# Optimization experiments

Hardware: AMD Instinct MI355X
Metric: run time of the kernel (lower is better)

Reference implementation:

```python
import jax, jax.numpy as jnp
import numpy as np

B, N_PER, D = 128, 512, 128        # graphs, nodes per graph, feature width
N = B * N_PER                      # 65536 total nodes
E = 524288                         # total edges (avg degree 8)
KS = (410, 328, 263)               # ceil(0.8*512), ceil(0.8*410), ceil(0.8*328)


def setup_inputs() -> dict:
    key = jax.random.key(0)
    ks = jax.random.split(key, 20)
    p = lambda k, shape: jax.random.normal(k, shape, jnp.float32) * 0.05
    rng = np.random.default_rng(0)
    g = rng.integers(0, B, size=E)
    s = rng.integers(0, N_PER, size=E)
    t = rng.integers(0, N_PER, size=E)
    edge_index = jnp.asarray(np.stack([g * N_PER + s, g * N_PER + t]).astype(np.int32))
    inp = {
        'x': jax.random.normal(ks[0], (N, 1, D), jnp.float32),
        'edge_index': edge_index,
    }
    i = 1
    for l in (1, 2, 3):
        inp[f'conv{l}_wl'] = p(ks[i], (D, D)); i += 1   # SAGEConv lin_l (neighbors) weight
        inp[f'conv{l}_bl'] = p(ks[i], (D,));  i += 1   # SAGEConv lin_l bias
        inp[f'conv{l}_wr'] = p(ks[i], (D, D)); i += 1   # SAGEConv lin_r (root) weight
        inp[f'pool{l}_w'] = p(ks[i], (D,));   i += 1   # TopKPooling score vector
    inp['lin1_w'] = p(ks[13], (128, 256)); inp['lin1_b'] = p(ks[14], (128,))
    inp['lin2_w'] = p(ks[15], (64, 128));  inp['lin2_b'] = p(ks[16], (64,))
    inp['lin3_w'] = p(ks[17], (1, 64));    inp['lin3_b'] = p(ks[18], (1,))
    return inp


def _sage(x, node_mask, src, dst, wl, bl, wr):
    # SAGEConv, mean aggregation: lin_l(mean_{j->i} x_j) + lin_r(x_i)
    em = (node_mask[src] & node_mask[dst]).astype(x.dtype)   # [E] valid-edge mask
    msum = jax.ops.segment_sum(x[src] * em[:, None], dst, num_segments=N)
    deg = jax.ops.segment_sum(em, dst, num_segments=N)
    mean = msum / jnp.maximum(deg, 1.0)[:, None]
    return mean @ wl.T + bl + x @ wr.T


def _topk_pool(x, node_mask, w, k):
    # TopKPooling: score = x.w/||w||; keep top-k per graph; gate kept x by tanh(score)
    score = (x @ w) / (jnp.linalg.norm(w) + 1e-16)           # [N]
    score = jnp.where(node_mask, score, -jnp.inf)
    _, idx = jax.lax.top_k(score.reshape(B, N_PER), k)       # [B, k] within-graph ids
    nm = jnp.zeros((B, N_PER), bool).at[jnp.arange(B)[:, None], idx].set(True).reshape(-1)
    x = jnp.where(nm[:, None], x * jnp.tanh(score)[:, None], 0.0)
    return x, nm


def _readout(x, node_mask, k):
    # cat([global_max_pool, global_mean_pool]) over the k surviving nodes per graph
    xb = x.reshape(B, N_PER, -1)
    mb = node_mask.reshape(B, N_PER, 1)
    gmax = jnp.max(jnp.where(mb, xb, -jnp.inf), axis=1)
    gmean = jnp.sum(jnp.where(mb, xb, 0.0), axis=1) / k
    return jnp.concatenate([gmax, gmean], axis=1)            # [B, 2D]


def _forward(edge_index, x, conv1_wl, conv1_bl, conv1_wr, pool1_w,
             conv2_wl, conv2_bl, conv2_wr, pool2_w,
             conv3_wl, conv3_bl, conv3_wr, pool3_w,
             lin1_w, lin1_b, lin2_w, lin2_b, lin3_w, lin3_b):
    src, dst = edge_index[0], edge_index[1]
    h = x[:, 0, :]                                           # x.squeeze(1) -> [N, D]
    nm = jnp.ones((N,), bool)
    layers = ((conv1_wl, conv1_bl, conv1_wr, pool1_w),
              (conv2_wl, conv2_bl, conv2_wr, pool2_w),
              (conv3_wl, conv3_bl, conv3_wr, pool3_w))
    reads = []
    for (wl, bl, wr, pw), k in zip(layers, KS):
        h = jax.nn.relu(_sage(h, nm, src, dst, wl, bl, wr))
        h, nm = _topk_pool(h, nm, pw, k)
        reads.append(_readout(h, nm, float(k)))
    z = reads[0] + reads[1] + reads[2]                       # [B, 256]
    z = jax.nn.relu(z @ lin1_w.T + lin1_b)
    z = jax.nn.relu(z @ lin2_w.T + lin2_b)
    # dropout p=0.5 is a no-op at eval time
    return jax.nn.sigmoid(z @ lin3_w.T + lin3_b)[:, 0]       # [B]


def reference(x, edge_index, conv1_wl, conv1_bl, conv1_wr, pool1_w,
              conv2_wl, conv2_bl, conv2_wr, pool2_w,
              conv3_wl, conv3_bl, conv3_wr, pool3_w,
              lin1_w, lin1_b, lin2_w, lin2_b, lin3_w, lin3_b):
    return _forward(edge_index, x, conv1_wl, conv1_bl, conv1_wr, pool1_w,
                    conv2_wl, conv2_bl, conv2_wr, pool2_w,
                    conv3_wl, conv3_bl, conv3_wr, pool3_w,
                    lin1_w, lin1_b, lin2_w, lin2_b, lin3_w, lin3_b)
```

## Files before the change

kernel.cpp:

```cpp
#include <hip/hip_runtime.h>
#include <math.h>

#define NND 65536
#define NPER 512
#define NGR 128
#define DD 128
#define NED 524288

typedef __attribute__((ext_vector_type(8))) short short8;
typedef __attribute__((ext_vector_type(4))) float f32x4;

__device__ __forceinline__ unsigned short f2b(float f) {
  unsigned u = __float_as_uint(f);
  return (unsigned short)((u + 0x7FFFu + ((u >> 16) & 1u)) >> 16);
}
__device__ __forceinline__ float b2f(unsigned short h) {
  return __uint_as_float(((unsigned)h) << 16);
}


__global__ __launch_bounds__(256) void init_prepw_kernel(
    int* __restrict__ counts, float2* __restrict__ tm,
    const float* __restrict__ wl0, const float* __restrict__ wr0,
    const float* __restrict__ wl1, const float* __restrict__ wr1,
    const float* __restrict__ wl2, const float* __restrict__ wr2,
    unsigned short* __restrict__ Whi, unsigned short* __restrict__ Wlo) {
  const int bid = blockIdx.x;
  if (bid < 256) {
    int i = bid * 256 + threadIdx.x;
    counts[i] = 0;
    tm[i] = make_float2(1.f, 1.f);
    return;
  }
  const float* wls[3] = {wl0, wl1, wl2};
  const float* wrs[3] = {wr0, wr1, wr2};
  int e = (bid - 256) * 256 + threadIdx.x;
  int l = e >> 15;
  int o = e & 32767;
  int j = o & 7;
  int lane = (o >> 3) & 63;
  int nt = (o >> 9) & 7;
  int kc = o >> 12;
  int li = lane & 15, q = lane >> 4;
  int n = nt * 16 + li;
  int k = kc * 32 + q * 8 + j;
  const float* src = (k < 128) ? wls[l] : wrs[l];
  float v = src[n * DD + (k & 127)];
  unsigned short hi = f2b(v);
  float lo = v - b2f(hi);
  Whi[e] = hi;
  Wlo[e] = f2b(lo);
}

__global__ __launch_bounds__(256) void hist_kernel(const int* __restrict__ ei,
                                                   int* __restrict__ counts) {
  int e = blockIdx.x * 256 + threadIdx.x;
  atomicAdd(&counts[ei[NED + e]], 1);
}


__global__ __launch_bounds__(256) void scan1_kernel(const int* __restrict__ counts,
                                                    int* __restrict__ csum) {
  __shared__ int ws[4];
  const int b = blockIdx.x;
  const int t = threadIdx.x;
  const int4 v = ((const int4*)(counts + b * 1024))[t];
  int s = v.x + v.y + v.z + v.w;
#pragma unroll
  for (int o = 32; o > 0; o >>= 1) s += __shfl_down(s, o);
  if ((t & 63) == 0) ws[t >> 6] = s;
  __syncthreads();
  if (t == 0) csum[b] = ws[0] + ws[1] + ws[2] + ws[3];
}

__global__ __launch_bounds__(256) void scan2_kernel(const int* __restrict__ counts,
                                                    const int* __restrict__ csum,
                                                    int* __restrict__ off,
                                                    int* __restrict__ cursor) {
  __shared__ int s_part[256];
  __shared__ int s_base;
  const int b = blockIdx.x;
  const int t = threadIdx.x;
  const int4 v = ((const int4*)(counts + b * 1024))[t];
  const int s = v.x + v.y + v.z + v.w;
  s_part[t] = s;
  if (t < 64) {
    int val = (t < b) ? csum[t] : 0;
#pragma unroll
    for (int o = 32; o > 0; o >>= 1) val += __shfl_down(val, o);
    if (t == 0) s_base = val;
  }
  __syncthreads();
  for (int d = 1; d < 256; d <<= 1) {
    int val = (t >= d) ? s_part[t - d] : 0;
    __syncthreads();
    s_part[t] += val;
    __syncthreads();
  }
  const int excl = s_base + ((t == 0) ? 0 : s_part[t - 1]);
  int4 o4;
  o4.x = excl;
  o4.y = excl + v.x;
  o4.z = o4.y + v.y;
  o4.w = o4.z + v.z;
  ((int4*)(off + b * 1024))[t] = o4;
  ((int4*)(cursor + b * 1024))[t] = o4;
  if (b == 0 && t == 0) off[NND] = NED;
}

__global__ __launch_bounds__(256) void scatter_kernel(const int* __restrict__ ei,
                                                      int* __restrict__ cursor,
                                                      int* __restrict__ ssrc) {
  int e = blockIdx.x * 256 + threadIdx.x;
  int dst = ei[NED + e];
  int pos = atomicAdd(&cursor[dst], 1);
  ssrc[pos] = ei[e];
}


template <int CM>
__global__ __launch_bounds__(256) void agg_kernel_t(const float* __restrict__ x,
                                                    const float2* __restrict__ tm,
                                                    const int* __restrict__ off,
                                                    const int* __restrict__ ssrc,
                                                    unsigned short* __restrict__ mhi,
                                                    unsigned short* __restrict__ mlo) {
  const int wave = threadIdx.x >> 6;
  const int lane = threadIdx.x & 63;
  const int half = lane >> 5;
  const int l = lane & 31;
  const int bid = blockIdx.x;
  const int xcd = bid & 7;
  const int slot = bid >> 3;
  const int graph = xcd * 16 + (slot >> 5);
  const int within = slot & 31;
  const int d0 = graph * NPER + within * 16 + wave * 4;

  int offv = 0;
  if (lane < 5) offv = off[d0 + lane];
  float deadv = 1.f;
  if (CM && lane < 4) deadv = tm[d0 + lane].x;
  const int b0 = __shfl(offv, 0);
  const int b1 = __shfl(offv, 1);
  const int b2 = __shfl(offv, 2);
  const int b3 = __shfl(offv, 3);
  const int e3 = __shfl(offv, 4);
  float dd[4];
  if (CM) {
    dd[0] = __shfl(deadv, 0);
    dd[1] = __shfl(deadv, 1);
    dd[2] = __shfl(deadv, 2);
    dd[3] = __shfl(deadv, 3);
  }
  const int begs[4] = {b0, b1, b2, b3};
  const int ends[4] = {b1, b2, b3, e3};

  float4 acc[4];
  int deg[4];
#pragma unroll
  for (int d = 0; d < 4; ++d) {
    acc[d] = make_float4(0.f, 0.f, 0.f, 0.f);
    deg[d] = 0;
  }

  for (int base = b0; base < e3; base += 64) {
    const int nwin = min(64, e3 - base);
    int sv = 0;
    float tv = 0.f;
    int live = 0;
    if (lane < nwin) {
      sv = ssrc[base + lane];
      if (CM) {
        const float2 mt = tm[sv];
        live = (mt.x != 0.f);
        tv = mt.y;
      }
    }
    unsigned long long bl;
    if (CM)
      bl = __ballot(live);
    else
      bl = (nwin == 64) ? ~0ull : ((1ull << nwin) - 1);

#pragma unroll
    for (int d = 0; d < 4; ++d) {
      if (CM && dd[d] == 0.f) continue;
      const int lo = max(begs[d], base);
      const int hi = min(ends[d], base + 64);
      if (lo >= hi) continue;
      const int j0 = lo - base;
      const int j1 = hi - base;
      const unsigned long long wm =
          (((j1 == 64) ? ~0ull : ((1ull << j1) - 1)) & ~((1ull << j0) - 1));
      deg[d] += (int)__popcll(bl & wm);
      int j = j0 + half;
      for (; j + 6 < j1; j += 8) {
        const int s0 = __shfl(sv, j);
        const int s1 = __shfl(sv, j + 2);
        const int s2 = __shfl(sv, j + 4);
        const int s3 = __shfl(sv, j + 6);
        const float4 v0 = *(const float4*)(x + (size_t)s0 * DD + l * 4);
        const float4 v1 = *(const float4*)(x + (size_t)s1 * DD + l * 4);
        const float4 v2 = *(const float4*)(x + (size_t)s2 * DD + l * 4);
        const float4 v3 = *(const float4*)(x + (size_t)s3 * DD + l * 4);
        if (CM) {
          const float t0 = __shfl(tv, j), t1 = __shfl(tv, j + 2);
          const float t2 = __shfl(tv, j + 4), t3 = __shfl(tv, j + 6);
          acc[d].x += v0.x * t0 + v1.x * t1 + v2.x * t2 + v3.x * t3;
          acc[d].y += v0.y * t0 + v1.y * t1 + v2.y * t2 + v3.y * t3;
          acc[d].z += v0.z * t0 + v1.z * t1 + v2.z * t2 + v3.z * t3;
          acc[d].w += v0.w * t0 + v1.w * t1 + v2.w * t2 + v3.w * t3;
        } else {
          acc[d].x += v0.x + v1.x + v2.x + v3.x;
          acc[d].y += v0.y + v1.y + v2.y + v3.y;
          acc[d].z += v0.z + v1.z + v2.z + v3.z;
          acc[d].w += v0.w + v1.w + v2.w + v3.w;
        }
      }
      for (; j < j1; j += 2) {
        const int s = __shfl(sv, j);
        const float4 v = *(const float4*)(x + (size_t)s * DD + l * 4);
        if (CM) {
          const float t = __shfl(tv, j);
          acc[d].x += v.x * t;
          acc[d].y += v.y * t;
          acc[d].z += v.z * t;
          acc[d].w += v.w * t;
        } else {
          acc[d].x += v.x;
          acc[d].y += v.y;
          acc[d].z += v.z;
          acc[d].w += v.w;
        }
      }
    }
  }

#pragma unroll
  for (int d = 0; d < 4; ++d) {
    float4 a = acc[d];
    a.x += __shfl(a.x, lane ^ 32);
    a.y += __shfl(a.y, lane ^ 32);
    a.z += __shfl(a.z, lane ^ 32);
    a.w += __shfl(a.w, lane ^ 32);
    if (lane < 32) {
      const float inv = 1.f / (float)max(deg[d], 1);
      float4 m;
      m.x = a.x * inv;
      m.y = a.y * inv;
      m.z = a.z * inv;
      m.w = a.w * inv;
      ushort4 hv, lv;
      hv.x = f2b(m.x); lv.x = f2b(m.x - b2f(hv.x));
      hv.y = f2b(m.y); lv.y = f2b(m.y - b2f(hv.y));
      hv.z = f2b(m.z); lv.z = f2b(m.z - b2f(hv.z));
      hv.w = f2b(m.w); lv.w = f2b(m.w - b2f(hv.w));
      const size_t ad = (size_t)(d0 + d) * DD + l * 4;
      *(ushort4*)(mhi + ad) = hv;
      *(ushort4*)(mlo + ad) = lv;
    }
  }
}


#define GBM 64

template <int SCALE>
__global__ __launch_bounds__(256) void gemm_kernel_t(
    const unsigned short* __restrict__ Amh, const unsigned short* __restrict__ Aml,
    const float* __restrict__ Ax, const float2* __restrict__ tmp,
    const unsigned short* __restrict__ Whi, const unsigned short* __restrict__ Wlo,
    const float* __restrict__ bias, const float* __restrict__ pw,
    float* __restrict__ outp, float* __restrict__ sraw) {
  __shared__ short Ah[4096];
  __shared__ short Al[4096];
  __shared__ float s_sp[4][GBM];
  const int tid = threadIdx.x;
  const int wv = tid >> 6;
  const int lane = tid & 63;
  const int q = lane >> 4;
  const int li = lane & 15;
  const int row0 = blockIdx.x * GBM;

  int sdst[2];
#pragma unroll
  for (int i = 0; i < 2; ++i) {
    const int id = tid + i * 256;
    const int r = id >> 3;
    const int kb = (id & 7) << 2;
    sdst[i] = ((r >> 4) * 64 + (kb >> 3) * 16 + (r & 15)) * 8 + (kb & 7);
  }

  f32x4 acc[4][2];
#pragma unroll
  for (int m = 0; m < 4; ++m)
#pragma unroll
    for (int n = 0; n < 2; ++n) acc[m][n] = (f32x4){0.f, 0.f, 0.f, 0.f};

  float4 pa[2];
  ushort4 pmh[2], pml[2];
  short8 pbh[2], pbl[2];

#define LOADA(KC)                                                                      \
  {                                                                                    \
    if ((KC) < 4) {                                                                    \
      const int cb = (KC)*32;                                                          \
      _Pragma("unroll") for (int i = 0; i < 2; ++i) {                                  \
        const int id = tid + i * 256;                                                  \
        const size_t ga = (size_t)(row0 + (id >> 3)) * DD + cb + ((id & 7) << 2);      \
        pmh[i] = *(const ushort4*)(Amh + ga);                                          \
        pml[i] = *(const ushort4*)(Aml + ga);                                          \
      }                                                                                \
    } else {                                                                           \
      const int cb = ((KC)&3) * 32;                                                    \
      _Pragma("unroll") for (int i = 0; i < 2; ++i) {                                  \
        const int id = tid + i * 256;                                                  \
        pa[i] = *(const float4*)(Ax + (size_t)(row0 + (id >> 3)) * DD + cb + ((id & 7) << 2)); \
        if (SCALE) {                                                                   \
          const float tt = tmp[row0 + (id >> 3)].y;                                    \
          pa[i].x *= tt; pa[i].y *= tt; pa[i].z *= tt; pa[i].w *= tt;                  \
        }                                                                              \
      }                                                                                \
    }                                                                                  \
  }
#define LOADB(KC)                                                                      \
  {                                                                                    \
    _Pragma("unroll") for (int n = 0; n < 2; ++n) {                                    \
      const int ga = (((KC)*8 + wv * 2 + n) * 64 + lane) * 8;                          \
      pbh[n] = *(const short8*)(Whi + ga);                                             \
      pbl[n] = *(const short8*)(Wlo + ga);                                             \
    }                                                                                  \
  }
#define STAGE(KC)                                                                      \
  {                                                                                    \
    short* Adh = Ah + ((KC)&1) * 2048;                                                 \
    short* Adl = Al + ((KC)&1) * 2048;                                                 \
    if ((KC) < 4) {                                                                    \
      _Pragma("unroll") for (int i = 0; i < 2; ++i) {                                  \
        *(ushort4*)(Adh + sdst[i]) = pmh[i];                                           \
        *(ushort4*)(Adl + sdst[i]) = pml[i];                                           \
      }                                                                                \
    } else {                                                                           \
      _Pragma("unroll") for (int i = 0; i < 2; ++i) {                                  \
        ushort4 hv, lv;                                                                \
        hv.x = f2b(pa[i].x); lv.x = f2b(pa[i].x - b2f(hv.x));                          \
        hv.y = f2b(pa[i].y); lv.y = f2b(pa[i].y - b2f(hv.y));                          \
        hv.z = f2b(pa[i].z); lv.z = f2b(pa[i].z - b2f(hv.z));                          \
        hv.w = f2b(pa[i].w); lv.w = f2b(pa[i].w - b2f(hv.w));                          \
        *(ushort4*)(Adh + sdst[i]) = hv;                                               \
        *(ushort4*)(Adl + sdst[i]) = lv;                                               \
      }                                                                                \
    }                                                                                  \
  }

  LOADA(0) LOADB(0)
  STAGE(0)
  LOADA(1)

#pragma unroll
  for (int kc = 0; kc < 8; ++kc) {
    short8 bh[2], bl[2];
    bh[0] = pbh[0]; bh[1] = pbh[1];
    bl[0] = pbl[0]; bl[1] = pbl[1];
    __syncthreads();
    short8 ah[4], al[4];
    const short* Ash = Ah + (kc & 1) * 2048;
    const short* Asl = Al + (kc & 1) * 2048;
#pragma unroll
    for (int m = 0; m < 4; ++m) {
      ah[m] = *(const short8*)(Ash + (m * 64 + lane) * 8);
      al[m] = *(const short8*)(Asl + (m * 64 + lane) * 8);
    }
    switch (kc) {
      case 0: STAGE(1) LOADB(1) LOADA(2) break;
      case 1: STAGE(2) LOADB(2) LOADA(3) break;
      case 2: STAGE(3) LOADB(3) LOADA(4) break;
      case 3: STAGE(4) LOADB(4) LOADA(5) break;
      case 4: STAGE(5) LOADB(5) LOADA(6) break;
      case 5: STAGE(6) LOADB(6) LOADA(7) break;
      case 6: STAGE(7) LOADB(7) break;
      default: break;
    }
#pragma unroll
    for (int m = 0; m < 4; ++m)
#pragma unroll
      for (int n = 0; n < 2; ++n) {
        acc[m][n] = __builtin_amdgcn_mfma_f32_16x16x32_bf16(ah[m], bh[n], acc[m][n], 0, 0, 0);
        acc[m][n] = __builtin_amdgcn_mfma_f32_16x16x32_bf16(ah[m], bl[n], acc[m][n], 0, 0, 0);
        acc[m][n] = __builtin_amdgcn_mfma_f32_16x16x32_bf16(al[m], bh[n], acc[m][n], 0, 0, 0);
      }
  }
#undef LOADA
#undef LOADB
#undef STAGE

  const int c0 = wv * 32 + li;
  const int c1 = wv * 32 + 16 + li;
  const float b0 = bias[c0], b1 = bias[c1];
  const float p0 = pw[c0], p1 = pw[c1];
  float sp[16];
#pragma unroll
  for (int m = 0; m < 4; ++m) {
#pragma unroll
    for (int i = 0; i < 4; ++i) {
      const int r = row0 + m * 16 + q * 4 + i;
      const float v0 = fmaxf(acc[m][0][i] + b0, 0.f);
      const float v1 = fmaxf(acc[m][1][i] + b1, 0.f);
      outp[(size_t)r * DD + c0] = v0;
      outp[(size_t)r * DD + c1] = v1;
      sp[m * 4 + i] = v0 * p0 + v1 * p1;
    }
  }
#pragma unroll
  for (int e = 0; e < 16; ++e) {
    sp[e] += __shfl_xor(sp[e], 1);
    sp[e] += __shfl_xor(sp[e], 2);
    sp[e] += __shfl_xor(sp[e], 4);
    sp[e] += __shfl_xor(sp[e], 8);
  }
  if (li == 0) {
#pragma unroll
    for (int e = 0; e < 16; ++e) s_sp[wv][(e >> 2) * 16 + q * 4 + (e & 3)] = sp[e];
  }
  __syncthreads();
  if (tid < GBM)
    sraw[row0 + tid] = s_sp[0][tid] + s_sp[1][tid] + s_sp[2][tid] + s_sp[3][tid];
}


__global__ __launch_bounds__(256) void pool_kernel(const float* __restrict__ h,
                                                   const float* __restrict__ sraw,
                                                   const float* __restrict__ pw,
                                                   const float2* __restrict__ tmP,
                                                   float2* __restrict__ tmN,
                                                   float* __restrict__ zp,
                                                   const int kk) {
  __shared__ float s_sc[NPER];
  __shared__ float s_t[128];
  __shared__ unsigned char s_sel[128];
  __shared__ int s_rk[256];
  __shared__ float4 red4[512];
  __shared__ float s_norm;
  const int b = blockIdx.x;
  const int g = b >> 2;
  const int q = b & 3;
  const int tid = threadIdx.x;
  const int lane = tid & 63;

  if (tid < 64) {
    const float v0 = pw[lane], v1 = pw[lane + 64];
    float p = v0 * v0 + v1 * v1;
#pragma unroll
    for (int o = 32; o > 0; o >>= 1) p += __shfl_down(p, o);
    if (lane == 0) s_norm = 1.f / (sqrtf(p) + 1e-16f);
  }
  __syncthreads();
  const float inv_norm = s_norm;
#pragma unroll
  for (int i = 0; i < 2; ++i) {
    const int n = tid + i * 256;
    const int node = g * NPER + n;
    s_sc[n] = (tmP[node].x != 0.f) ? sraw[node] * inv_norm : -INFINITY;
  }
  __syncthreads();

  {
    const int n = q * 128 + (tid & 127);
    const int jb = (tid >> 7) * 256;
    const float s = s_sc[n];
    int rank = 0;
    for (int j = jb; j < jb + 256; ++j) {
      const float sj = s_sc[j];
      rank += (sj > s || (sj == s && j < n)) ? 1 : 0;
    }
    s_rk[tid] = rank;
  }
  __syncthreads();
  if (tid < 128) {
    const int n = q * 128 + tid;
    const int rank = s_rk[tid] + s_rk[tid + 128];
    const int sel = (rank < kk) ? 1 : 0;
    const float s = s_sc[n];
    const float t = sel ? tanhf(s) : 0.f;
    tmN[g * NPER + n] = make_float2(sel ? 1.f : 0.f, t);
    s_sel[tid] = (unsigned char)sel;
    s_t[tid] = t;
  }
  __syncthreads();

  const int c = tid & 31;
  const int r = tid >> 5;
  float4 pmax = make_float4(-INFINITY, -INFINITY, -INFINITY, -INFINITY);
  float4 psum = make_float4(0.f, 0.f, 0.f, 0.f);
  const size_t nbase = (size_t)g * NPER + q * 128;
  const float4* h4 = (const float4*)h;
  for (int i = 0; i < 16; ++i) {
    const int nl = r + 8 * i;
    if (s_sel[nl]) {
      float4 v = h4[(nbase + nl) * 32 + c];
      const float t = s_t[nl];
      v.x *= t; v.y *= t; v.z *= t; v.w *= t;
      pmax.x = fmaxf(pmax.x, v.x);
      pmax.y = fmaxf(pmax.y, v.y);
      pmax.z = fmaxf(pmax.z, v.z);
      pmax.w = fmaxf(pmax.w, v.w);
      psum.x += v.x; psum.y += v.y; psum.z += v.z; psum.w += v.w;
    }
  }
  red4[r * 32 + c] = pmax;
  red4[256 + r * 32 + c] = psum;
  __syncthreads();
  if (tid < 32) {
    float4 m = red4[tid];
    float4 sm = red4[256 + tid];
#pragma unroll
    for (int rr = 1; rr < 8; ++rr) {
      const float4 a = red4[rr * 32 + tid];
      const float4 s2 = red4[256 + rr * 32 + tid];
      m.x = fmaxf(m.x, a.x); m.y = fmaxf(m.y, a.y);
      m.z = fmaxf(m.z, a.z); m.w = fmaxf(m.w, a.w);
      sm.x += s2.x; sm.y += s2.y; sm.z += s2.z; sm.w += s2.w;
    }
    *(float4*)(zp + (size_t)b * 256 + tid * 4) = m;
    *(float4*)(zp + (size_t)b * 256 + 128 + tid * 4) = sm;
  }
}


__global__ __launch_bounds__(128) void mlp_kernel(const float* __restrict__ zpart,
                                                  const float* __restrict__ w1,
                                                  const float* __restrict__ b1,
                                                  const float* __restrict__ w2,
                                                  const float* __restrict__ b2,
                                                  const float* __restrict__ w3,
                                                  const float* __restrict__ b3,
                                                  float* __restrict__ out,
                                                  const float ik0, const float ik1,
                                                  const float ik2) {
  __shared__ float z[256];
  __shared__ float h1[128];
  __shared__ float h2[64];
  const int g = blockIdx.x;
  const int t = threadIdx.x;
  const float iks[3] = {ik0, ik1, ik2};
  float zmax = 0.f, zmean = 0.f;
#pragma unroll
  for (int l = 0; l < 3; ++l) {
    const float* zp = zpart + ((size_t)l * 512 + g * 4) * 256;
    zmax += fmaxf(fmaxf(zp[t], zp[256 + t]), fmaxf(zp[512 + t], zp[768 + t]));
    zmean += (zp[128 + t] + zp[384 + t] + zp[640 + t] + zp[896 + t]) * iks[l];
  }
  z[t] = zmax;
  z[128 + t] = zmean;
  __syncthreads();
  float a = b1[t];
  for (int k = 0; k < 256; ++k) a = fmaf(z[k], w1[t * 256 + k], a);
  h1[t] = fmaxf(a, 0.f);
  __syncthreads();
  if (t < 64) {
    float a2 = b2[t];
    for (int k = 0; k < 128; ++k) a2 = fmaf(h1[k], w2[t * 128 + k], a2);
    h2[t] = fmaxf(a2, 0.f);
  }
  __syncthreads();
  if (t == 0) {
    float a3 = b3[0];
    for (int k = 0; k < 64; ++k) a3 = fmaf(h2[k], w3[k], a3);
    out[g] = 1.f / (1.f + expf(-a3));
  }
}


extern "C" void kernel_launch(void* const* d_in, const int* in_sizes, int n_in,
                              void* d_out, int out_size, void* d_ws, size_t ws_size,
                              hipStream_t stream) {
  (void)in_sizes; (void)n_in; (void)out_size; (void)ws_size;
  const float* x_in = (const float*)d_in[0];
  const int* ei = (const int*)d_in[1];
  const float* wl[3] = {(const float*)d_in[2], (const float*)d_in[6], (const float*)d_in[10]};
  const float* cbl[3] = {(const float*)d_in[3], (const float*)d_in[7], (const float*)d_in[11]};
  const float* wr[3] = {(const float*)d_in[4], (const float*)d_in[8], (const float*)d_in[12]};
  const float* pw[3] = {(const float*)d_in[5], (const float*)d_in[9], (const float*)d_in[13]};
  const float* l1w = (const float*)d_in[14];
  const float* l1b = (const float*)d_in[15];
  const float* l2w = (const float*)d_in[16];
  const float* l2b = (const float*)d_in[17];
  const float* l3w = (const float*)d_in[18];
  const float* l3b = (const float*)d_in[19];
  float* out = (float*)d_out;

  char* w = (char*)d_ws;
  int* counts = (int*)(w + 0 * (1 << 20));
  int* off = (int*)(w + 1 * (1 << 20));
  int* csum = (int*)(w + 1 * (1 << 20) + (1 << 19));
  int* cursor = (int*)(w + 2 * (1 << 20));
  float* sraw = (float*)(w + 2 * (1 << 20));
  float2* tmA = (float2*)(w + 3 * (1 << 20));
  float2* tmB = (float2*)(w + 3 * (1 << 20) + (1 << 19));
  float* zpart = (float*)(w + 4 * (1 << 20));
  unsigned short* Whi = (unsigned short*)(w + 5 * (1 << 20) + (1 << 19));
  unsigned short* Wlo = (unsigned short*)(w + 5 * (1 << 20) + 3 * (1 << 18));
  int* ssrc = (int*)(w + 6 * (1 << 20));
  unsigned short* mhi = (unsigned short*)(w + (size_t)8 * (1 << 20));
  unsigned short* mlo = (unsigned short*)(w + (size_t)24 * (1 << 20));
  float* hA = (float*)(w + (size_t)40 * (1 << 20));
  float* hB = (float*)(w + (size_t)72 * (1 << 20));

  init_prepw_kernel<<<640, 256, 0, stream>>>(counts, tmA, wl[0], wr[0], wl[1], wr[1],
                                             wl[2], wr[2], Whi, Wlo);
  hist_kernel<<<NED / 256, 256, 0, stream>>>(ei, counts);
  scan1_kernel<<<64, 256, 0, stream>>>(counts, csum);
  scan2_kernel<<<64, 256, 0, stream>>>(counts, csum, off, cursor);
  scatter_kernel<<<NED / 256, 256, 0, stream>>>(ei, cursor, ssrc);

  const int ks[3] = {410, 328, 263};
  const float* xl = x_in;
  float* houts[3] = {hA, hB, hA};
  float2* tprev[3] = {tmA, tmB, tmA};
  float2* tnext[3] = {tmB, tmA, tmB};
  for (int l = 0; l < 3; ++l) {
    float* hout = houts[l];
    if (l == 0) {
      agg_kernel_t<0><<<4096, 256, 0, stream>>>(xl, tprev[l], off, ssrc, mhi, mlo);
      gemm_kernel_t<0><<<NND / GBM, 256, 0, stream>>>(mhi, mlo, xl, tprev[l],
                                                      Whi + (size_t)l * 32768,
                                                      Wlo + (size_t)l * 32768, cbl[l], pw[l],
                                                      hout, sraw);
    } else {
      agg_kernel_t<1><<<4096, 256, 0, stream>>>(xl, tprev[l], off, ssrc, mhi, mlo);
      gemm_kernel_t<1><<<NND / GBM, 256, 0, stream>>>(mhi, mlo, xl, tprev[l],
                                                      Whi + (size_t)l * 32768,
                                                      Wlo + (size_t)l * 32768, cbl[l], pw[l],
                                                      hout, sraw);
    }
    pool_kernel<<<NGR * 4, 256, 0, stream>>>(hout, sraw, pw[l], tprev[l], tnext[l],
                                             zpart + (size_t)l * 512 * 256, ks[l]);
    xl = hout;
  }
  mlp_kernel<<<NGR, 128, 0, stream>>>(zpart, l1w, l1b, l2w, l2b, l3w, l3b, out,
                                      1.f / 410.f, 1.f / 328.f, 1.f / 263.f);
}
```

Baseline: 362.9 us.

## Stage per-graph feature half-tile in LDS for neighbor aggregation

The aggregation kernel now assigns one 1024-thread block to each graph and half of the feature columns. It loads that graph's 512x64 feature slab, the mask/tanh table and the CSR offsets into shared memory, then gathers neighbor rows from LDS instead of global memory, relying on edges staying within a graph (the source index is masked to a local id). This removes scattered global gathers, but uses about 132KB of LDS per block, launches only 256 blocks, and each lane accumulates a single scalar column, so occupancy and parallelism drop.

```diff
diff --git a/kernel.cpp b/kernel.cpp
--- a/kernel.cpp
+++ b/kernel.cpp
@@ -119,146 +119,104 @@
 
 
 template <int CM>
-__global__ __launch_bounds__(256) void agg_kernel_t(const float* __restrict__ x,
-                                                    const float2* __restrict__ tm,
-                                                    const int* __restrict__ off,
-                                                    const int* __restrict__ ssrc,
-                                                    unsigned short* __restrict__ mhi,
-                                                    unsigned short* __restrict__ mlo) {
-  const int wave = threadIdx.x >> 6;
-  const int lane = threadIdx.x & 63;
-  const int half = lane >> 5;
-  const int l = lane & 31;
-  const int bid = blockIdx.x;
-  const int xcd = bid & 7;
-  const int slot = bid >> 3;
-  const int graph = xcd * 16 + (slot >> 5);
-  const int within = slot & 31;
-  const int d0 = graph * NPER + within * 16 + wave * 4;
-
-  int offv = 0;
-  if (lane < 5) offv = off[d0 + lane];
-  float deadv = 1.f;
-  if (CM && lane < 4) deadv = tm[d0 + lane].x;
-  const int b0 = __shfl(offv, 0);
-  const int b1 = __shfl(offv, 1);
-  const int b2 = __shfl(offv, 2);
-  const int b3 = __shfl(offv, 3);
-  const int e3 = __shfl(offv, 4);
-  float dd[4];
+__global__ __launch_bounds__(1024) void agg_kernel_t(const float* __restrict__ x,
+                                                     const float2* __restrict__ tm,
+                                                     const int* __restrict__ off,
+                                                     const int* __restrict__ ssrc,
+                                                     unsigned short* __restrict__ mhi,
+                                                     unsigned short* __restrict__ mlo) {
+  __shared__ float xs[NPER * 64];
+  __shared__ float2 tms[NPER];
+  __shared__ int soff[NPER + 1];
+  const int b = blockIdx.x;
+  const int g = b >> 1;
+  const int colbase = (b & 1) << 6;
+  const int tid = threadIdx.x;
+  const int lane = tid & 63;
+  const int w = tid >> 6;
+  const int nbase = g * NPER;
+
+  {
+    const int row = tid >> 4;
+    const int c4 = (tid & 15) << 2;
+#pragma unroll
+    for (int r = 0; r < NPER; r += 64) {
+      const float4 v =
+          *(const float4*)(x + (size_t)(nbase + row + r) * DD + colbase + c4);
+      *(float4*)(xs + (row + r) * 64 + c4) = v;
+    }
+  }
   if (CM) {
-    dd[0] = __shfl(deadv, 0);
-    dd[1] = __shfl(deadv, 1);
-    dd[2] = __shfl(deadv, 2);
-    dd[3] = __shfl(deadv, 3);
-  }
-  const int begs[4] = {b0, b1, b2, b3};
-  const int ends[4] = {b1, b2, b3, e3};
-
-  float4 acc[4];
-  int deg[4];
-#pragma unroll
-  for (int d = 0; d < 4; ++d) {
-    acc[d] = make_float4(0.f, 0.f, 0.f, 0.f);
-    deg[d] = 0;
-  }
-
-  for (int base = b0; base < e3; base += 64) {
-    const int nwin = min(64, e3 - base);
-    int sv = 0;
-    float tv = 0.f;
-    int live = 0;
-    if (lane < nwin) {
-      sv = ssrc[base + lane];
-      if (CM) {
-        const float2 mt = tm[sv];
-        live = (mt.x != 0.f);
-        tv = mt.y;
-      }
-    }
-    unsigned long long bl;
-    if (CM)
-      bl = __ballot(live);
-    else
-      bl = (nwin == 64) ? ~0ull : ((1ull << nwin) - 1);
-
-#pragma unroll
-    for (int d = 0; d < 4; ++d) {
-      if (CM && dd[d] == 0.f) continue;
-      const int lo = max(begs[d], base);
-      const int hi = min(ends[d], base + 64);
-      if (lo >= hi) continue;
-      const int j0 = lo - base;
-      const int j1 = hi - base;
-      const unsigned long long wm =
-          (((j1 == 64) ? ~0ull : ((1ull << j1) - 1)) & ~((1ull << j0) - 1));
-      deg[d] += (int)__popcll(bl & wm);
-      int j = j0 + half;
-      for (; j + 6 < j1; j += 8) {
-        const int s0 = __shfl(sv, j);
-        const int s1 = __shfl(sv, j + 2);
-        const int s2 = __shfl(sv, j + 4);
-        const int s3 = __shfl(sv, j + 6);
-        const float4 v0 = *(const float4*)(x + (size_t)s0 * DD + l * 4);
-        const float4 v1 = *(const float4*)(x + (size_t)s1 * DD + l * 4);
-        const float4 v2 = *(const float4*)(x + (size_t)s2 * DD + l * 4);
-        const float4 v3 = *(const float4*)(x + (size_t)s3 * DD + l * 4);
+    if (tid < NPER) tms[tid] = tm[nbase + tid];
+  }
+  if (tid < NPER + 1) soff[tid] = off[nbase + tid];
+  __syncthreads();
+
+  const float* xl = xs + lane;
+  for (int i = 0; i < 32; ++i) {
+    const int n = w * 32 + i;
+    if (CM && tms[n].x == 0.f) continue;
+    const int beg = soff[n];
+    const int end = soff[n + 1];
+    float acc = 0.f;
+    int deg = 0;
+    for (int base = beg; base < end; base += 64) {
+      const int cnt = min(64, end - base);
+      int sv = 0;
+      float tv = 0.f;
+      int live = 0;
+      if (lane < cnt) {
+        sv = (ssrc[base + lane] & (NPER - 1)) << 6;
         if (CM) {
-          const float t0 = __shfl(tv, j), t1 = __shfl(tv, j + 2);
-          const float t2 = __shfl(tv, j + 4), t3 = __shfl(tv, j + 6);
-          acc[d].x += v0.x * t0 + v1.x * t1 + v2.x * t2 + v3.x * t3;
-          acc[d].y += v0.y * t0 + v1.y * t1 + v2.y * t2 + v3.y * t3;
-          acc[d].z += v0.z * t0 + v1.z * t1 + v2.z * t2 + v3.z * t3;
-          acc[d].w += v0.w * t0 + v1.w * t1 + v2.w * t2 + v3.w * t3;
-        } else {
-          acc[d].x += v0.x + v1.x + v2.x + v3.x;
-          acc[d].y += v0.y + v1.y + v2.y + v3.y;
-          acc[d].z += v0.z + v1.z + v2.z + v3.z;
-          acc[d].w += v0.w + v1.w + v2.w + v3.w;
+          const float2 mt = tms[sv >> 6];
+          live = (mt.x != 0.f);
+          tv = mt.y;
         }
       }
-      for (; j < j1; j += 2) {
-        const int s = __shfl(sv, j);
-        const float4 v = *(const float4*)(x + (size_t)s * DD + l * 4);
-        if (CM) {
+      if (CM)
+        deg += (int)__popcll(__ballot(live));
+      else
+        deg += cnt;
+      int j = 0;
+      if (CM) {
+        for (; j + 3 < cnt; j += 4) {
+          const int s0 = __shfl(sv, j), s1 = __shfl(sv, j + 1);
+          const int s2 = __shfl(sv, j + 2), s3 = __shfl(sv, j + 3);
+          const float t0 = __shfl(tv, j), t1 = __shfl(tv, j + 1);
+          const float t2 = __shfl(tv, j + 2), t3 = __shfl(tv, j + 3);
+          const float v0 = xl[s0], v1 = xl[s1], v2 = xl[s2], v3 = xl[s3];
+          acc += v0 * t0;
+          acc += v1 * t1;
+          acc += v2 * t2;
+          acc += v3 * t3;
+        }
+        for (; j < cnt; ++j) {
+          const int s = __shfl(sv, j);
           const float t = __shfl(tv, j);
-          acc[d].x += v.x * t;
-          acc[d].y += v.y * t;
-          acc[d].z += v.z * t;
-          acc[d].w += v.w * t;
-        } else {
-          acc[d].x += v.x;
-          acc[d].y += v.y;
-          acc[d].z += v.z;
-          acc[d].w += v.w;
+          acc += xl[s] * t;
+        }
+      } else {
+        for (; j + 3 < cnt; j += 4) {
+          const int s0 = __shfl(sv, j), s1 = __shfl(sv, j + 1);
+          const int s2 = __shfl(sv, j + 2), s3 = __shfl(sv, j + 3);
+          const float v0 = xl[s0], v1 = xl[s1], v2 = xl[s2], v3 = xl[s3];
+          acc += v0;
+          acc += v1;
+          acc += v2;
+          acc += v3;
+        }
+        for (; j < cnt; ++j) {
+          const int s = __shfl(sv, j);
+          acc += xl[s];
         }
       }
     }
-  }
-
-#pragma unroll
-  for (int d = 0; d < 4; ++d) {
-    float4 a = acc[d];
-    a.x += __shfl(a.x, lane ^ 32);
-    a.y += __shfl(a.y, lane ^ 32);
-    a.z += __shfl(a.z, lane ^ 32);
-    a.w += __shfl(a.w, lane ^ 32);
-    if (lane < 32) {
-      const float inv = 1.f / (float)max(deg[d], 1);
-      float4 m;
-      m.x = a.x * inv;
-      m.y = a.y * inv;
-      m.z = a.z * inv;
-      m.w = a.w * inv;
-      ushort4 hv, lv;
-      hv.x = f2b(m.x); lv.x = f2b(m.x - b2f(hv.x));
-      hv.y = f2b(m.y); lv.y = f2b(m.y - b2f(hv.y));
-      hv.z = f2b(m.z); lv.z = f2b(m.z - b2f(hv.z));
-      hv.w = f2b(m.w); lv.w = f2b(m.w - b2f(hv.w));
-      const size_t ad = (size_t)(d0 + d) * DD + l * 4;
-      *(ushort4*)(mhi + ad) = hv;
-      *(ushort4*)(mlo + ad) = lv;
-    }
+    const float m = acc * (1.f / (float)max(deg, 1));
+    const unsigned short hv = f2b(m);
+    const unsigned short lv = f2b(m - b2f(hv));
+    const size_t ad = (size_t)(nbase + n) * DD + colbase + lane;
+    mhi[ad] = hv;
+    mlo[ad] = lv;
   }
 }
 
@@ -621,13 +579,13 @@
   for (int l = 0; l < 3; ++l) {
     float* hout = houts[l];
     if (l == 0) {
-      agg_kernel_t<0><<<4096, 256, 0, stream>>>(xl, tprev[l], off, ssrc, mhi, mlo);
+      agg_kernel_t<0><<<NGR * 2, 1024, 0, stream>>>(xl, tprev[l], off, ssrc, mhi, mlo);
       gemm_kernel_t<0><<<NND / GBM, 256, 0, stream>>>(mhi, mlo, xl, tprev[l],
                                                       Whi + (size_t)l * 32768,
                                                       Wlo + (size_t)l * 32768, cbl[l], pw[l],
                                                       hout, sraw);
     } else {
-      agg_kernel_t<1><<<4096, 256, 0, stream>>>(xl, tprev[l], off, ssrc, mhi, mlo);
+      agg_kernel_t<1><<<NGR * 2, 1024, 0, stream>>>(xl, tprev[l], off, ssrc, mhi, mlo);
       gemm_kernel_t<1><<<NND / GBM, 256, 0, stream>>>(mhi, mlo, xl, tprev[l],
                                                       Whi + (size_t)l * 32768,
                                                       Wlo + (size_t)l * 32768, cbl[l], pw[l],
```

Result: slower. 405.3 us (+11.7%).
